# Optimization experiments

Measured on AMD Instinct MI355X. Metric: run time of the kernel, lower is better.

The kernel has to match this reference:

```python
import jax, jax.numpy as jnp
import numpy as np

G, N, F, H, L, B = 8, 1024, 128, 256, 4, 64


def setup_inputs() -> dict:
    key = jax.random.key(0)
    ks = jax.random.split(key, 8)
    graph = jax.random.randint(ks[0], (B,), 0, G)
    # boolean coverpoint mask; force column 0 True so no row is empty
    mask = jax.random.uniform(ks[1], (B, N)) < 0.2
    mask = mask.at[:, 0].set(True)
    cdfg_xs = jax.random.normal(ks[2], (G, N, F), dtype=jnp.float32)
    cdfg_as = (jax.random.uniform(ks[3], (G, N, N)) < 0.02).astype(jnp.float32) / 20.0
    W_in = jax.random.normal(ks[4], (F, H), dtype=jnp.float32) * (1.0 / np.sqrt(F))
    b_in = jnp.zeros((H,), dtype=jnp.float32)
    Ws = jax.random.normal(ks[5], (L, H, H), dtype=jnp.float32) * (1.0 / np.sqrt(H))
    bs = jnp.zeros((L, H), dtype=jnp.float32)
    return {"graph": graph, "coverpoint_mask": mask, "cdfg_xs": cdfg_xs,
            "cdfg_as": cdfg_as, "W_in": W_in, "b_in": b_in, "Ws": Ws, "bs": bs}


def reference(graph, coverpoint_mask, cdfg_xs, cdfg_as, W_in, b_in, Ws, bs):
    # gather per-sample graphs (tf.gather_nd equivalent)
    xs = cdfg_xs[graph]          # [B, N, F]
    As = cdfg_as[graph]          # [B, N, N]
    # input Dense with relu
    x = jax.nn.relu(jnp.einsum('bnf,fh->bnh', xs, W_in) + b_in)  # [B, N, H]
    to_add = x
    n_layers = Ws.shape[0]
    for i in range(n_layers):
        h = jnp.einsum('bnm,bmh->bnh', As, jnp.einsum('bnh,hk->bnk', x, Ws[i])) + bs[i]
        if i == n_layers - 1:
            x = jax.nn.softmax(h, axis=-1)   # final_activation='softmax'
        else:
            x = jax.nn.relu(h)
    x = x + to_add
    # ragged boolean_mask + reduce_mean over nodes == masked mean
    m = coverpoint_mask[..., None].astype(x.dtype)   # [B, N, 1]
    s = jnp.sum(x * m, axis=1)                       # [B, H]
    cnt = jnp.maximum(jnp.sum(m, axis=1), 1.0)
    return s / cnt
```

## Files before the change

### kernel.cpp

```cpp
#include <hip/hip_runtime.h>
#include <hip/hip_bf16.h>

#define GG 8
#define NN 1024
#define FF 128
#define HH 256
#define LL 4
#define BB 64
#define MM (GG * NN)
#define ELLCAP 96

typedef __attribute__((ext_vector_type(8))) short bf16x8_t;
typedef __attribute__((ext_vector_type(4))) float f32x4_t;

__device__ inline unsigned short f2bf(float f) {
  union { float f; unsigned u; } c;
  c.f = f;
  unsigned r = (c.u + 0x7fffu + ((c.u >> 16) & 1u)) >> 16;
  return (unsigned short)r;
}
__device__ inline float bf2f(unsigned short u) {
  union { unsigned u; float f; } c;
  c.u = (unsigned)u << 16;
  return c.f;
}

#define PB_DET 16
#define PB_XS (PB_DET + 1024)
#define PB_W (PB_XS + 1152)
#define PB_ELL (PB_W + 2048)
__global__ __launch_bounds__(256) void prep_kernel(
    const uint4* __restrict__ mask4, int* __restrict__ flags,
    const float4* __restrict__ xs4, ushort4* __restrict__ xsb4,
    const float* __restrict__ W_in, const float* __restrict__ Ws,
    unsigned short* __restrict__ WinT, unsigned short* __restrict__ WsT,
    const float* __restrict__ Adj, uint2* __restrict__ ell,
    int* __restrict__ cntArr) {
  const int bx = blockIdx.x;
  if (bx < PB_DET) {
    const int i = bx * 256 + threadIdx.x;
    const uint4 v = mask4[i];
    const unsigned all = v.x | v.y | v.z | v.w;
    const int nonz = (all & 0xFFFFFF00u) != 0;
    const int isf32 = ((v.x >> 24) == 0x3fu) || ((v.y >> 24) == 0x3fu) ||
                      ((v.z >> 24) == 0x3fu) || ((v.w >> 24) == 0x3fu);
    const unsigned long long bn = __ballot(nonz);
    const unsigned long long bf = __ballot(isf32);
    if ((threadIdx.x & 63) == 0) {
      if (bn) atomicOr(&flags[0], 1);
      if (bf) atomicOr(&flags[1], 1);
    }
  } else if (bx < PB_XS) {
    const int i = (bx - PB_DET) * 256 + threadIdx.x;
    const float4 v = xs4[i];
    ushort4 o;
    o.x = f2bf(v.x); o.y = f2bf(v.y); o.z = f2bf(v.z); o.w = f2bf(v.w);
    xsb4[i] = o;
  } else if (bx < PB_W) {
    const int idx = (bx - PB_XS) * 256 + threadIdx.x;
    if (idx < FF * HH) {
      const int n = idx >> 7, k = idx & (FF - 1);
      WinT[idx] = f2bf(W_in[k * HH + n]);
    } else {
      const int j = idx - FF * HH;
      const int l = j >> 16, n = (j >> 8) & 255, k = j & 255;
      WsT[j] = f2bf(Ws[((size_t)l * HH + k) * HH + n]);
    }
  } else {
    const int lane = threadIdx.x & 63;
    const int wid = threadIdx.x >> 6;
    const int r = (bx - PB_W) * 4 + wid;
    const float* __restrict__ Arow = Adj + (size_t)r * NN;
    int cnt = 0;
    for (int mc = 0; mc < NN; mc += 64) {
      const float a = Arow[mc + lane];
      const unsigned long long bal = __ballot(a != 0.0f);
      if (a != 0.0f) {
        const int pos = cnt + __popcll(bal & ((1ULL << lane) - 1ULL));
        if (pos < ELLCAP) {
          uint2 e;
          e.x = __float_as_uint(a);
          e.y = (unsigned)(mc + lane);
          ell[(size_t)r * ELLCAP + pos] = e;
        }
      }
      cnt += __popcll(bal);
    }
    if (lane == 0) cntArr[r] = min(cnt, ELLCAP);
  }
}

template <int K, bool FUSED>
__global__ __launch_bounds__(256) void mfma_gemm_kernel(
    const unsigned short* __restrict__ A, const unsigned short* __restrict__ BT,
    const float* __restrict__ bias, unsigned short* __restrict__ Cb,
    float* __restrict__ Cf) {
  constexpr int KS = K / 8;
  __shared__ uint4 As4[64 * KS];
  __shared__ uint4 Bs4[64 * KS];
  const int t = threadIdx.x;
  const int lane = t & 63;
  const int w = t >> 6;
  const int wm = (w >> 1) * 32;
  const int wn = (w & 1) * 32;
  const int m0 = blockIdx.x * 64;
  const int n0 = blockIdx.y * 64;
  const int lk = lane >> 4;
  const int lr = lane & 15;
  const uint4* __restrict__ Ag = (const uint4*)(A + (size_t)m0 * K);
  const uint4* __restrict__ Bg = (const uint4*)(BT + (size_t)n0 * K);
#pragma unroll
  for (int it = 0; it < K / 32; ++it) {
    const int c = it * 256 + t;
    const int row = c / KS;
    const int k = c % KS;
    const int slot = row * KS + (k ^ (row & 7));
    As4[slot] = Ag[c];
    Bs4[slot] = Bg[c];
  }
  __syncthreads();
  f32x4_t acc[2][2] = {};
#pragma unroll
  for (int ks = 0; ks < K / 32; ++ks) {
    const int q = ks * 4 + lk;
    const int ra0 = wm + lr, ra1 = wm + 16 + lr;
    const int rb0 = wn + lr, rb1 = wn + 16 + lr;
    const bf16x8_t a0 = *(const bf16x8_t*)(&As4[ra0 * KS + (q ^ (ra0 & 7))]);
    const bf16x8_t a1 = *(const bf16x8_t*)(&As4[ra1 * KS + (q ^ (ra1 & 7))]);
    const bf16x8_t b0 = *(const bf16x8_t*)(&Bs4[rb0 * KS + (q ^ (rb0 & 7))]);
    const bf16x8_t b1 = *(const bf16x8_t*)(&Bs4[rb1 * KS + (q ^ (rb1 & 7))]);
    acc[0][0] = __builtin_amdgcn_mfma_f32_16x16x32_bf16(a0, b0, acc[0][0], 0, 0, 0);
    acc[0][1] = __builtin_amdgcn_mfma_f32_16x16x32_bf16(a0, b1, acc[0][1], 0, 0, 0);
    acc[1][0] = __builtin_amdgcn_mfma_f32_16x16x32_bf16(a1, b0, acc[1][0], 0, 0, 0);
    acc[1][1] = __builtin_amdgcn_mfma_f32_16x16x32_bf16(a1, b1, acc[1][1], 0, 0, 0);
  }
#pragma unroll
  for (int rg = 0; rg < 2; ++rg)
#pragma unroll
    for (int cg = 0; cg < 2; ++cg)
#pragma unroll
      for (int j = 0; j < 4; ++j) {
        const int row = m0 + wm + rg * 16 + (lane >> 4) * 4 + j;
        const int col = n0 + wn + cg * 16 + lr;
        float v = acc[rg][cg][j];
        if (FUSED) {
          v += bias[col];
          v = fmaxf(v, 0.0f);
          Cb[(size_t)row * HH + col] = f2bf(v);
          Cf[(size_t)row * HH + col] = v;
        } else {
          Cb[(size_t)row * HH + col] = f2bf(v);
        }
      }
}

__global__ __launch_bounds__(256) void spmm_ell_kernel(
    const uint2* __restrict__ ell, const int* __restrict__ cntArr,
    const unsigned short* __restrict__ Yb, const float* __restrict__ bias,
    const float* __restrict__ X0, unsigned short* __restrict__ Xb,
    float* __restrict__ Xf, int final_layer) {
  const int lane = threadIdx.x & 63;
  const int wid = threadIdx.x >> 6;
  const int r = blockIdx.x * 4 + wid;
  const int g = r >> 10;
  const unsigned short* __restrict__ Yg = Yb + (size_t)g * NN * HH;
  const int cnt = cntArr[r];
  const uint2* __restrict__ erow = ell + (size_t)r * ELLCAP;
  float p0 = 0.f, p1 = 0.f, p2 = 0.f, p3 = 0.f;
  float q0 = 0.f, q1 = 0.f, q2 = 0.f, q3 = 0.f;
  for (int base = 0; base < cnt; base += 64) {
    const int m = min(64, cnt - base);
    const uint2 e = erow[base + ((lane < m) ? lane : 0)];
    int j = 0;
    for (; j + 2 <= m; j += 2) {
      const float v0 = __uint_as_float(__shfl(e.x, j));
      const int i0 = (int)__shfl(e.y, j);
      const float v1 = __uint_as_float(__shfl(e.x, j + 1));
      const int i1 = (int)__shfl(e.y, j + 1);
      const ushort4 y0 = *(const ushort4*)(Yg + (size_t)i0 * HH + lane * 4);
      const ushort4 y1 = *(const ushort4*)(Yg + (size_t)i1 * HH + lane * 4);
      p0 += v0 * bf2f(y0.x); p1 += v0 * bf2f(y0.y);
      p2 += v0 * bf2f(y0.z); p3 += v0 * bf2f(y0.w);
      q0 += v1 * bf2f(y1.x); q1 += v1 * bf2f(y1.y);
      q2 += v1 * bf2f(y1.z); q3 += v1 * bf2f(y1.w);
    }
    if (j < m) {
      const float v0 = __uint_as_float(__shfl(e.x, j));
      const int i0 = (int)__shfl(e.y, j);
      const ushort4 y0 = *(const ushort4*)(Yg + (size_t)i0 * HH + lane * 4);
      p0 += v0 * bf2f(y0.x); p1 += v0 * bf2f(y0.y);
      p2 += v0 * bf2f(y0.z); p3 += v0 * bf2f(y0.w);
    }
  }
  const float4 b4 = *(const float4*)(bias + lane * 4);
  const float h0 = p0 + q0 + b4.x, h1 = p1 + q1 + b4.y;
  const float h2 = p2 + q2 + b4.z, h3 = p3 + q3 + b4.w;
  const size_t rowoff = (size_t)r * HH;
  if (!final_layer) {
    ushort4 o;
    o.x = f2bf(fmaxf(h0, 0.f));
    o.y = f2bf(fmaxf(h1, 0.f));
    o.z = f2bf(fmaxf(h2, 0.f));
    o.w = f2bf(fmaxf(h3, 0.f));
    *(ushort4*)(Xb + rowoff + lane * 4) = o;
  } else {
    float mx = fmaxf(fmaxf(h0, h1), fmaxf(h2, h3));
#pragma unroll
    for (int off = 32; off >= 1; off >>= 1) mx = fmaxf(mx, __shfl_xor(mx, off));
    const float e0 = __expf(h0 - mx), e1 = __expf(h1 - mx);
    const float e2 = __expf(h2 - mx), e3 = __expf(h3 - mx);
    float s = e0 + e1 + e2 + e3;
#pragma unroll
    for (int off = 32; off >= 1; off >>= 1) s += __shfl_xor(s, off);
    const float inv = 1.0f / s;
    const float4 x0 = *(const float4*)(X0 + rowoff + lane * 4);
    float4 o;
    o.x = e0 * inv + x0.x;
    o.y = e1 * inv + x0.y;
    o.z = e2 * inv + x0.z;
    o.w = e3 * inv + x0.w;
    *(float4*)(Xf + rowoff + lane * 4) = o;
  }
}

__global__ __launch_bounds__(256) void mm_partial_kernel(
    const float* __restrict__ X, const int* __restrict__ graph,
    const void* __restrict__ mask, const int* __restrict__ flags,
    float* __restrict__ partial, float* __restrict__ cntbuf) {
  __shared__ unsigned char m[64];
  const int c = blockIdx.x;
  const int b = blockIdx.y;
  const int h = threadIdx.x;
  const int n0 = c * 64;
  const int mode = flags[1] ? 2 : (flags[0] ? 0 : 1);
  if (h < 64) {
    const int n = n0 + h;
    bool on;
    if (mode == 1) on = ((const int*)mask)[(size_t)b * NN + n] != 0;
    else if (mode == 2) on = ((const float*)mask)[(size_t)b * NN + n] != 0.0f;
    else on = ((const unsigned char*)mask)[(size_t)b * NN + n] != 0;
    m[h] = on ? 1 : 0;
  }
  __syncthreads();
  const int g = graph[b];
  const float* __restrict__ Xg = X + ((size_t)g * NN + n0) * HH;
  float a0 = 0.f, a1 = 0.f, a2 = 0.f, a3 = 0.f;
  int c0 = 0, c1 = 0, c2 = 0, c3 = 0;
#pragma unroll 4
  for (int n = 0; n < 16; ++n) {
    if (m[n])      { a0 += Xg[(size_t)n * HH + h]; c0++; }
    if (m[n + 16]) { a1 += Xg[(size_t)(n + 16) * HH + h]; c1++; }
    if (m[n + 32]) { a2 += Xg[(size_t)(n + 32) * HH + h]; c2++; }
    if (m[n + 48]) { a3 += Xg[(size_t)(n + 48) * HH + h]; c3++; }
  }
  partial[((size_t)b * 16 + c) * HH + h] = (a0 + a1) + (a2 + a3);
  if (h == 0) cntbuf[b * 16 + c] = (float)((c0 + c1) + (c2 + c3));
}

__global__ __launch_bounds__(256) void mm_reduce_kernel(
    const float* __restrict__ partial, const float* __restrict__ cntbuf,
    float* __restrict__ out) {
  const int b = blockIdx.x, h = threadIdx.x;
  float s = 0.f;
#pragma unroll
  for (int c = 0; c < 16; ++c) s += partial[((size_t)b * 16 + c) * HH + h];
  float cnt = 0.f;
#pragma unroll
  for (int c = 0; c < 16; ++c) cnt += cntbuf[b * 16 + c];
  out[(size_t)b * HH + h] = s / fmaxf(cnt, 1.0f);
}

extern "C" void kernel_launch(void* const* d_in, const int* in_sizes, int n_in,
                              void* d_out, int out_size, void* d_ws,
                              size_t ws_size, hipStream_t stream) {
  const int* graph = (const int*)d_in[0];
  const void* mask = d_in[1];
  const float* xs = (const float*)d_in[2];
  const float* As = (const float*)d_in[3];
  const float* W_in = (const float*)d_in[4];
  const float* b_in = (const float*)d_in[5];
  const float* Ws = (const float*)d_in[6];
  const float* bs = (const float*)d_in[7];
  float* out = (float*)d_out;

  float* X = (float*)d_ws;
  float* X0 = X + (size_t)MM * HH;
  unsigned short* Yb = (unsigned short*)(X0 + (size_t)MM * HH);
  unsigned short* Xb = Yb + (size_t)MM * HH;
  unsigned short* xsb = Xb + (size_t)MM * HH;
  unsigned short* WinT = xsb + (size_t)MM * FF;
  unsigned short* WsT = WinT + (size_t)HH * FF;
  uint2* ell = (uint2*)(WsT + (size_t)LL * HH * HH);
  int* cntArr = (int*)(ell + (size_t)MM * ELLCAP);
  int* flags = cntArr + MM;
  float* partial = (float*)(flags + 2);
  float* cntbuf = partial + (size_t)BB * 16 * HH;

  hipMemsetAsync(flags, 0, 2 * sizeof(int), stream);
  prep_kernel<<<PB_ELL, 256, 0, stream>>>(
      (const uint4*)mask, flags, (const float4*)xs, (ushort4*)xsb, W_in, Ws,
      WinT, WsT, As, ell, cntArr);

  const dim3 grd(MM / 64, HH / 64);
  mfma_gemm_kernel<FF, true><<<grd, 256, 0, stream>>>(xsb, WinT, b_in, Xb, X0);
  for (int i = 0; i < LL; ++i) {
    mfma_gemm_kernel<HH, false><<<grd, 256, 0, stream>>>(
        Xb, WsT + (size_t)i * HH * HH, nullptr, Yb, nullptr);
    spmm_ell_kernel<<<MM / 4, 256, 0, stream>>>(
        ell, cntArr, Yb, bs + (size_t)i * HH, X0, Xb, X, (i == LL - 1) ? 1 : 0);
  }
  mm_partial_kernel<<<dim3(16, BB), 256, 0, stream>>>(X, graph, mask, flags,
                                                      partial, cntbuf);
  mm_reduce_kernel<<<BB, 256, 0, stream>>>(partial, cntbuf, out);
}
```

Baseline: 185.5 us.

## Fuse all stages into one cooperative persistent kernel with grid syncs

Replaces the sequence of separate launches (prep, input GEMM, per-layer GEMM and SpMM, masked-mean partial and reduce, plus a memset) with a single cooperative kernel of 256 persistent blocks. The blocks loop over virtual tiles and use grid-wide syncs between stages. Mask-type detection now runs in one block with shared-memory flags instead of global atomics across 16 blocks. This removes launch gaps and the memset, but with only 256 blocks the GEMM and SpMM stages get less parallelism and occupancy, since 64KB of shared memory per block limits residency. It also adds the cost of the grid barriers.

```diff
diff --git a/kernel.cpp b/kernel.cpp
--- a/kernel.cpp
+++ b/kernel.cpp
@@ -1,5 +1,7 @@
 #include <hip/hip_runtime.h>
-#include <hip/hip_bf16.h>
+#include <hip/hip_cooperative_groups.h>
+
+namespace cg = cooperative_groups;
 
 #define GG 8
 #define NN 1024
@@ -9,6 +11,12 @@
 #define BB 64
 #define MM (GG * NN)
 #define ELLCAP 96
+#define NBLK 256
+
+#define PB_DET 1
+#define PB_XS (PB_DET + 1024)
+#define PB_W (PB_XS + 1152)
+#define PB_TOT (PB_W + 2048)
 
 typedef __attribute__((ext_vector_type(8))) short bf16x8_t;
 typedef __attribute__((ext_vector_type(4))) float f32x4_t;
@@ -25,90 +33,51 @@
   return c.f;
 }
 
-#define PB_DET 16
-#define PB_XS (PB_DET + 1024)
-#define PB_W (PB_XS + 1152)
-#define PB_ELL (PB_W + 2048)
-__global__ __launch_bounds__(256) void prep_kernel(
-    const uint4* __restrict__ mask4, int* __restrict__ flags,
-    const float4* __restrict__ xs4, ushort4* __restrict__ xsb4,
-    const float* __restrict__ W_in, const float* __restrict__ Ws,
-    unsigned short* __restrict__ WinT, unsigned short* __restrict__ WsT,
-    const float* __restrict__ Adj, uint2* __restrict__ ell,
-    int* __restrict__ cntArr) {
-  const int bx = blockIdx.x;
-  if (bx < PB_DET) {
-    const int i = bx * 256 + threadIdx.x;
-    const uint4 v = mask4[i];
-    const unsigned all = v.x | v.y | v.z | v.w;
-    const int nonz = (all & 0xFFFFFF00u) != 0;
-    const int isf32 = ((v.x >> 24) == 0x3fu) || ((v.y >> 24) == 0x3fu) ||
-                      ((v.z >> 24) == 0x3fu) || ((v.w >> 24) == 0x3fu);
-    const unsigned long long bn = __ballot(nonz);
-    const unsigned long long bf = __ballot(isf32);
-    if ((threadIdx.x & 63) == 0) {
-      if (bn) atomicOr(&flags[0], 1);
-      if (bf) atomicOr(&flags[1], 1);
-    }
-  } else if (bx < PB_XS) {
-    const int i = (bx - PB_DET) * 256 + threadIdx.x;
-    const float4 v = xs4[i];
-    ushort4 o;
-    o.x = f2bf(v.x); o.y = f2bf(v.y); o.z = f2bf(v.z); o.w = f2bf(v.w);
-    xsb4[i] = o;
-  } else if (bx < PB_W) {
-    const int idx = (bx - PB_XS) * 256 + threadIdx.x;
-    if (idx < FF * HH) {
-      const int n = idx >> 7, k = idx & (FF - 1);
-      WinT[idx] = f2bf(W_in[k * HH + n]);
-    } else {
-      const int j = idx - FF * HH;
-      const int l = j >> 16, n = (j >> 8) & 255, k = j & 255;
-      WsT[j] = f2bf(Ws[((size_t)l * HH + k) * HH + n]);
-    }
-  } else {
-    const int lane = threadIdx.x & 63;
-    const int wid = threadIdx.x >> 6;
-    const int r = (bx - PB_W) * 4 + wid;
-    const float* __restrict__ Arow = Adj + (size_t)r * NN;
-    int cnt = 0;
-    for (int mc = 0; mc < NN; mc += 64) {
-      const float a = Arow[mc + lane];
-      const unsigned long long bal = __ballot(a != 0.0f);
-      if (a != 0.0f) {
-        const int pos = cnt + __popcll(bal & ((1ULL << lane) - 1ULL));
-        if (pos < ELLCAP) {
-          uint2 e;
-          e.x = __float_as_uint(a);
-          e.y = (unsigned)(mc + lane);
-          ell[(size_t)r * ELLCAP + pos] = e;
-        }
-      }
-      cnt += __popcll(bal);
-    }
-    if (lane == 0) cntArr[r] = min(cnt, ELLCAP);
-  }
-}
+struct KParams {
+  const int* graph;
+  const void* mask;
+  const float* xs;
+  const float* Adj;
+  const float* W_in;
+  const float* b_in;
+  const float* Ws;
+  const float* bs;
+  float* out;
+  float* X;
+  float* X0;
+  unsigned short* Yb;
+  unsigned short* Xb;
+  unsigned short* xsb;
+  unsigned short* WinT;
+  unsigned short* WsT;
+  uint2* ell;
+  int* cntArr;
+  int* flags;
+  float* partial;
+  float* cntbuf;
+};
 
 template <int K, bool FUSED>
-__global__ __launch_bounds__(256) void mfma_gemm_kernel(
-    const unsigned short* __restrict__ A, const unsigned short* __restrict__ BT,
-    const float* __restrict__ bias, unsigned short* __restrict__ Cb,
-    float* __restrict__ Cf) {
+__device__ inline void gemm_tile(const unsigned short* __restrict__ A,
+                                 const unsigned short* __restrict__ BT,
+                                 const float* __restrict__ bias,
+                                 unsigned short* __restrict__ Cb,
+                                 float* __restrict__ Cf, uint4* smem, int vt,
+                                 int t) {
   constexpr int KS = K / 8;
-  __shared__ uint4 As4[64 * KS];
-  __shared__ uint4 Bs4[64 * KS];
-  const int t = threadIdx.x;
+  uint4* As4 = smem;
+  uint4* Bs4 = smem + 64 * KS;
   const int lane = t & 63;
   const int w = t >> 6;
   const int wm = (w >> 1) * 32;
   const int wn = (w & 1) * 32;
-  const int m0 = blockIdx.x * 64;
-  const int n0 = blockIdx.y * 64;
+  const int m0 = (vt >> 2) * 64;
+  const int n0 = (vt & 3) * 64;
   const int lk = lane >> 4;
   const int lr = lane & 15;
   const uint4* __restrict__ Ag = (const uint4*)(A + (size_t)m0 * K);
   const uint4* __restrict__ Bg = (const uint4*)(BT + (size_t)n0 * K);
+  __syncthreads();
 #pragma unroll
   for (int it = 0; it < K / 32; ++it) {
     const int c = it * 256 + t;
@@ -154,162 +123,228 @@
       }
 }
 
-__global__ __launch_bounds__(256) void spmm_ell_kernel(
-    const uint2* __restrict__ ell, const int* __restrict__ cntArr,
-    const unsigned short* __restrict__ Yb, const float* __restrict__ bias,
-    const float* __restrict__ X0, unsigned short* __restrict__ Xb,
-    float* __restrict__ Xf, int final_layer) {
-  const int lane = threadIdx.x & 63;
-  const int wid = threadIdx.x >> 6;
-  const int r = blockIdx.x * 4 + wid;
-  const int g = r >> 10;
-  const unsigned short* __restrict__ Yg = Yb + (size_t)g * NN * HH;
-  const int cnt = cntArr[r];
-  const uint2* __restrict__ erow = ell + (size_t)r * ELLCAP;
-  float p0 = 0.f, p1 = 0.f, p2 = 0.f, p3 = 0.f;
-  float q0 = 0.f, q1 = 0.f, q2 = 0.f, q3 = 0.f;
-  for (int base = 0; base < cnt; base += 64) {
-    const int m = min(64, cnt - base);
-    const uint2 e = erow[base + ((lane < m) ? lane : 0)];
-    int j = 0;
-    for (; j + 2 <= m; j += 2) {
-      const float v0 = __uint_as_float(__shfl(e.x, j));
-      const int i0 = (int)__shfl(e.y, j);
-      const float v1 = __uint_as_float(__shfl(e.x, j + 1));
-      const int i1 = (int)__shfl(e.y, j + 1);
-      const ushort4 y0 = *(const ushort4*)(Yg + (size_t)i0 * HH + lane * 4);
-      const ushort4 y1 = *(const ushort4*)(Yg + (size_t)i1 * HH + lane * 4);
-      p0 += v0 * bf2f(y0.x); p1 += v0 * bf2f(y0.y);
-      p2 += v0 * bf2f(y0.z); p3 += v0 * bf2f(y0.w);
-      q0 += v1 * bf2f(y1.x); q1 += v1 * bf2f(y1.y);
-      q2 += v1 * bf2f(y1.z); q3 += v1 * bf2f(y1.w);
+__global__ __launch_bounds__(256) void fused_kernel(KParams p) {
+  cg::grid_group grid = cg::this_grid();
+  __shared__ uint4 smem[4096];
+  const int bid = blockIdx.x;
+  const int t = threadIdx.x;
+  const int lane = t & 63;
+  const int wid = t >> 6;
+
+  for (int vb = bid; vb < PB_TOT; vb += NBLK) {
+    if (vb == 0) {
+      int* df = (int*)smem;
+      if (t < 2) df[t] = 0;
+      __syncthreads();
+      int nonz = 0, isf = 0;
+      const uint4* mask4 = (const uint4*)p.mask;
+      for (int i = t; i < 4096; i += 256) {
+        const uint4 v = mask4[i];
+        const unsigned all = v.x | v.y | v.z | v.w;
+        if (all & 0xFFFFFF00u) nonz = 1;
+        if (((v.x >> 24) == 0x3fu) || ((v.y >> 24) == 0x3fu) ||
+            ((v.z >> 24) == 0x3fu) || ((v.w >> 24) == 0x3fu))
+          isf = 1;
+      }
+      if (nonz) atomicOr(&df[0], 1);
+      if (isf) atomicOr(&df[1], 1);
+      __syncthreads();
+      if (t == 0) p.flags[0] = df[1] ? 2 : (df[0] ? 0 : 1);
+      __syncthreads();
+    } else if (vb < PB_XS) {
+      const int i = (vb - PB_DET) * 256 + t;
+      const float4 v = ((const float4*)p.xs)[i];
+      ushort4 o;
+      o.x = f2bf(v.x); o.y = f2bf(v.y); o.z = f2bf(v.z); o.w = f2bf(v.w);
+      ((ushort4*)p.xsb)[i] = o;
+    } else if (vb < PB_W) {
+      const int idx = (vb - PB_XS) * 256 + t;
+      if (idx < FF * HH) {
+        const int n = idx >> 7, k = idx & (FF - 1);
+        p.WinT[idx] = f2bf(p.W_in[k * HH + n]);
+      } else {
+        const int j = idx - FF * HH;
+        const int l = j >> 16, n = (j >> 8) & 255, k = j & 255;
+        p.WsT[j] = f2bf(p.Ws[((size_t)l * HH + k) * HH + n]);
+      }
+    } else {
+      const int r = (vb - PB_W) * 4 + wid;
+      const float* __restrict__ Arow = p.Adj + (size_t)r * NN;
+      int cnt = 0;
+      for (int mc = 0; mc < NN; mc += 64) {
+        const float a = Arow[mc + lane];
+        const unsigned long long bal = __ballot(a != 0.0f);
+        if (a != 0.0f) {
+          const int pos = cnt + __popcll(bal & ((1ULL << lane) - 1ULL));
+          if (pos < ELLCAP) {
+            uint2 e;
+            e.x = __float_as_uint(a);
+            e.y = (unsigned)(mc + lane);
+            p.ell[(size_t)r * ELLCAP + pos] = e;
+          }
+        }
+        cnt += __popcll(bal);
+      }
+      if (lane == 0) p.cntArr[r] = min(cnt, ELLCAP);
     }
-    if (j < m) {
-      const float v0 = __uint_as_float(__shfl(e.x, j));
-      const int i0 = (int)__shfl(e.y, j);
-      const ushort4 y0 = *(const ushort4*)(Yg + (size_t)i0 * HH + lane * 4);
-      p0 += v0 * bf2f(y0.x); p1 += v0 * bf2f(y0.y);
-      p2 += v0 * bf2f(y0.z); p3 += v0 * bf2f(y0.w);
+  }
+  grid.sync();
+
+  for (int vt = bid; vt < 512; vt += NBLK)
+    gemm_tile<FF, true>(p.xsb, p.WinT, p.b_in, p.Xb, p.X0, smem, vt, t);
+  grid.sync();
+
+  for (int i = 0; i < LL; ++i) {
+    for (int vt = bid; vt < 512; vt += NBLK)
+      gemm_tile<HH, false>(p.Xb, p.WsT + (size_t)i * HH * HH, nullptr, p.Yb,
+                           nullptr, smem, vt, t);
+    grid.sync();
+    {
+      const int fin = (i == LL - 1);
+      const float* __restrict__ bias = p.bs + (size_t)i * HH;
+      for (int vt = bid; vt < 2048; vt += NBLK) {
+        const int r = vt * 4 + wid;
+        const int g = r >> 10;
+        const unsigned short* __restrict__ Yg = p.Yb + (size_t)g * NN * HH;
+        const int cnt = p.cntArr[r];
+        const uint2* __restrict__ erow = p.ell + (size_t)r * ELLCAP;
+        float p0 = 0.f, p1 = 0.f, p2 = 0.f, p3 = 0.f;
+        float q0 = 0.f, q1 = 0.f, q2 = 0.f, q3 = 0.f;
+        for (int base = 0; base < cnt; base += 64) {
+          const int m = min(64, cnt - base);
+          const uint2 e = erow[base + ((lane < m) ? lane : 0)];
+          int j = 0;
+          for (; j + 2 <= m; j += 2) {
+            const float v0 = __uint_as_float(__shfl(e.x, j));
+            const int i0 = (int)__shfl(e.y, j);
+            const float v1 = __uint_as_float(__shfl(e.x, j + 1));
+            const int i1 = (int)__shfl(e.y, j + 1);
+            const ushort4 y0 =
+                *(const ushort4*)(Yg + (size_t)i0 * HH + (lane << 2));
+            const ushort4 y1 =
+                *(const ushort4*)(Yg + (size_t)i1 * HH + (lane << 2));
+            p0 += v0 * bf2f(y0.x); p1 += v0 * bf2f(y0.y);
+            p2 += v0 * bf2f(y0.z); p3 += v0 * bf2f(y0.w);
+            q0 += v1 * bf2f(y1.x); q1 += v1 * bf2f(y1.y);
+            q2 += v1 * bf2f(y1.z); q3 += v1 * bf2f(y1.w);
+          }
+          if (j < m) {
+            const float v0 = __uint_as_float(__shfl(e.x, j));
+            const int i0 = (int)__shfl(e.y, j);
+            const ushort4 y0 =
+                *(const ushort4*)(Yg + (size_t)i0 * HH + (lane << 2));
+            p0 += v0 * bf2f(y0.x); p1 += v0 * bf2f(y0.y);
+            p2 += v0 * bf2f(y0.z); p3 += v0 * bf2f(y0.w);
+          }
+        }
+        const float4 b4 = *(const float4*)(bias + (lane << 2));
+        const float h0 = p0 + q0 + b4.x, h1 = p1 + q1 + b4.y;
+        const float h2 = p2 + q2 + b4.z, h3 = p3 + q3 + b4.w;
+        const size_t rowoff = (size_t)r * HH;
+        if (!fin) {
+          ushort4 o;
+          o.x = f2bf(fmaxf(h0, 0.f));
+          o.y = f2bf(fmaxf(h1, 0.f));
+          o.z = f2bf(fmaxf(h2, 0.f));
+          o.w = f2bf(fmaxf(h3, 0.f));
+          *(ushort4*)(p.Xb + rowoff + (lane << 2)) = o;
+        } else {
+          float mx = fmaxf(fmaxf(h0, h1), fmaxf(h2, h3));
+#pragma unroll
+          for (int off = 32; off >= 1; off >>= 1)
+            mx = fmaxf(mx, __shfl_xor(mx, off));
+          const float e0 = __expf(h0 - mx), e1 = __expf(h1 - mx);
+          const float e2 = __expf(h2 - mx), e3 = __expf(h3 - mx);
+          float s = e0 + e1 + e2 + e3;
+#pragma unroll
+          for (int off = 32; off >= 1; off >>= 1) s += __shfl_xor(s, off);
+          const float inv = 1.0f / s;
+          const float4 x0 = *(const float4*)(p.X0 + rowoff + (lane << 2));
+          float4 o;
+          o.x = e0 * inv + x0.x;
+          o.y = e1 * inv + x0.y;
+          o.z = e2 * inv + x0.z;
+          o.w = e3 * inv + x0.w;
+          *(float4*)(p.X + rowoff + (lane << 2)) = o;
+        }
+      }
     }
-  }
-  const float4 b4 = *(const float4*)(bias + lane * 4);
-  const float h0 = p0 + q0 + b4.x, h1 = p1 + q1 + b4.y;
-  const float h2 = p2 + q2 + b4.z, h3 = p3 + q3 + b4.w;
-  const size_t rowoff = (size_t)r * HH;
-  if (!final_layer) {
-    ushort4 o;
-    o.x = f2bf(fmaxf(h0, 0.f));
-    o.y = f2bf(fmaxf(h1, 0.f));
-    o.z = f2bf(fmaxf(h2, 0.f));
-    o.w = f2bf(fmaxf(h3, 0.f));
-    *(ushort4*)(Xb + rowoff + lane * 4) = o;
-  } else {
-    float mx = fmaxf(fmaxf(h0, h1), fmaxf(h2, h3));
-#pragma unroll
-    for (int off = 32; off >= 1; off >>= 1) mx = fmaxf(mx, __shfl_xor(mx, off));
-    const float e0 = __expf(h0 - mx), e1 = __expf(h1 - mx);
-    const float e2 = __expf(h2 - mx), e3 = __expf(h3 - mx);
-    float s = e0 + e1 + e2 + e3;
-#pragma unroll
-    for (int off = 32; off >= 1; off >>= 1) s += __shfl_xor(s, off);
-    const float inv = 1.0f / s;
-    const float4 x0 = *(const float4*)(X0 + rowoff + lane * 4);
-    float4 o;
-    o.x = e0 * inv + x0.x;
-    o.y = e1 * inv + x0.y;
-    o.z = e2 * inv + x0.z;
-    o.w = e3 * inv + x0.w;
-    *(float4*)(Xf + rowoff + lane * 4) = o;
-  }
-}
-
-__global__ __launch_bounds__(256) void mm_partial_kernel(
-    const float* __restrict__ X, const int* __restrict__ graph,
-    const void* __restrict__ mask, const int* __restrict__ flags,
-    float* __restrict__ partial, float* __restrict__ cntbuf) {
-  __shared__ unsigned char m[64];
-  const int c = blockIdx.x;
-  const int b = blockIdx.y;
-  const int h = threadIdx.x;
-  const int n0 = c * 64;
-  const int mode = flags[1] ? 2 : (flags[0] ? 0 : 1);
-  if (h < 64) {
-    const int n = n0 + h;
-    bool on;
-    if (mode == 1) on = ((const int*)mask)[(size_t)b * NN + n] != 0;
-    else if (mode == 2) on = ((const float*)mask)[(size_t)b * NN + n] != 0.0f;
-    else on = ((const unsigned char*)mask)[(size_t)b * NN + n] != 0;
-    m[h] = on ? 1 : 0;
-  }
-  __syncthreads();
-  const int g = graph[b];
-  const float* __restrict__ Xg = X + ((size_t)g * NN + n0) * HH;
-  float a0 = 0.f, a1 = 0.f, a2 = 0.f, a3 = 0.f;
-  int c0 = 0, c1 = 0, c2 = 0, c3 = 0;
+    grid.sync();
+  }
+
+  {
+    unsigned char* m = (unsigned char*)smem;
+    const int mode = p.flags[0];
+    for (int vb = bid; vb < 16 * BB; vb += NBLK) {
+      const int c = vb & 15, b = vb >> 4;
+      const int n0 = c * 64;
+      __syncthreads();
+      if (t < 64) {
+        const int n = n0 + t;
+        bool on;
+        if (mode == 1) on = ((const int*)p.mask)[(size_t)b * NN + n] != 0;
+        else if (mode == 2) on = ((const float*)p.mask)[(size_t)b * NN + n] != 0.0f;
+        else on = ((const unsigned char*)p.mask)[(size_t)b * NN + n] != 0;
+        m[t] = on ? 1 : 0;
+      }
+      __syncthreads();
+      const int g = p.graph[b];
+      const float* __restrict__ Xg = p.X + ((size_t)g * NN + n0) * HH;
+      float a0 = 0.f, a1 = 0.f, a2 = 0.f, a3 = 0.f;
+      int c0 = 0, c1 = 0, c2 = 0, c3 = 0;
 #pragma unroll 4
-  for (int n = 0; n < 16; ++n) {
-    if (m[n])      { a0 += Xg[(size_t)n * HH + h]; c0++; }
-    if (m[n + 16]) { a1 += Xg[(size_t)(n + 16) * HH + h]; c1++; }
-    if (m[n + 32]) { a2 += Xg[(size_t)(n + 32) * HH + h]; c2++; }
-    if (m[n + 48]) { a3 += Xg[(size_t)(n + 48) * HH + h]; c3++; }
-  }
-  partial[((size_t)b * 16 + c) * HH + h] = (a0 + a1) + (a2 + a3);
-  if (h == 0) cntbuf[b * 16 + c] = (float)((c0 + c1) + (c2 + c3));
-}
-
-__global__ __launch_bounds__(256) void mm_reduce_kernel(
-    const float* __restrict__ partial, const float* __restrict__ cntbuf,
-    float* __restrict__ out) {
-  const int b = blockIdx.x, h = threadIdx.x;
-  float s = 0.f;
-#pragma unroll
-  for (int c = 0; c < 16; ++c) s += partial[((size_t)b * 16 + c) * HH + h];
-  float cnt = 0.f;
-#pragma unroll
-  for (int c = 0; c < 16; ++c) cnt += cntbuf[b * 16 + c];
-  out[(size_t)b * HH + h] = s / fmaxf(cnt, 1.0f);
+      for (int n = 0; n < 16; ++n) {
+        if (m[n])      { a0 += Xg[(size_t)n * HH + t]; c0++; }
+        if (m[n + 16]) { a1 += Xg[(size_t)(n + 16) * HH + t]; c1++; }
+        if (m[n + 32]) { a2 += Xg[(size_t)(n + 32) * HH + t]; c2++; }
+        if (m[n + 48]) { a3 += Xg[(size_t)(n + 48) * HH + t]; c3++; }
+      }
+      p.partial[((size_t)b * 16 + c) * HH + t] = (a0 + a1) + (a2 + a3);
+      if (t == 0) p.cntbuf[b * 16 + c] = (float)((c0 + c1) + (c2 + c3));
+    }
+  }
+  grid.sync();
+
+  if (bid < BB) {
+    const int b = bid;
+    float s = 0.f;
+#pragma unroll
+    for (int c = 0; c < 16; ++c) s += p.partial[((size_t)b * 16 + c) * HH + t];
+    float cnt = 0.f;
+#pragma unroll
+    for (int c = 0; c < 16; ++c) cnt += p.cntbuf[b * 16 + c];
+    p.out[(size_t)b * HH + t] = s / fmaxf(cnt, 1.0f);
+  }
 }
 
 extern "C" void kernel_launch(void* const* d_in, const int* in_sizes, int n_in,
                               void* d_out, int out_size, void* d_ws,
                               size_t ws_size, hipStream_t stream) {
-  const int* graph = (const int*)d_in[0];
-  const void* mask = d_in[1];
-  const float* xs = (const float*)d_in[2];
-  const float* As = (const float*)d_in[3];
-  const float* W_in = (const float*)d_in[4];
-  const float* b_in = (const float*)d_in[5];
-  const float* Ws = (const float*)d_in[6];
-  const float* bs = (const float*)d_in[7];
-  float* out = (float*)d_out;
-
-  float* X = (float*)d_ws;
-  float* X0 = X + (size_t)MM * HH;
-  unsigned short* Yb = (unsigned short*)(X0 + (size_t)MM * HH);
-  unsigned short* Xb = Yb + (size_t)MM * HH;
-  unsigned short* xsb = Xb + (size_t)MM * HH;
-  unsigned short* WinT = xsb + (size_t)MM * FF;
-  unsigned short* WsT = WinT + (size_t)HH * FF;
-  uint2* ell = (uint2*)(WsT + (size_t)LL * HH * HH);
-  int* cntArr = (int*)(ell + (size_t)MM * ELLCAP);
-  int* flags = cntArr + MM;
-  float* partial = (float*)(flags + 2);
-  float* cntbuf = partial + (size_t)BB * 16 * HH;
-
-  hipMemsetAsync(flags, 0, 2 * sizeof(int), stream);
-  prep_kernel<<<PB_ELL, 256, 0, stream>>>(
-      (const uint4*)mask, flags, (const float4*)xs, (ushort4*)xsb, W_in, Ws,
-      WinT, WsT, As, ell, cntArr);
-
-  const dim3 grd(MM / 64, HH / 64);
-  mfma_gemm_kernel<FF, true><<<grd, 256, 0, stream>>>(xsb, WinT, b_in, Xb, X0);
-  for (int i = 0; i < LL; ++i) {
-    mfma_gemm_kernel<HH, false><<<grd, 256, 0, stream>>>(
-        Xb, WsT + (size_t)i * HH * HH, nullptr, Yb, nullptr);
-    spmm_ell_kernel<<<MM / 4, 256, 0, stream>>>(
-        ell, cntArr, Yb, bs + (size_t)i * HH, X0, Xb, X, (i == LL - 1) ? 1 : 0);
-  }
-  mm_partial_kernel<<<dim3(16, BB), 256, 0, stream>>>(X, graph, mask, flags,
-                                                      partial, cntbuf);
-  mm_reduce_kernel<<<BB, 256, 0, stream>>>(partial, cntbuf, out);
-}
+  KParams p;
+  p.graph = (const int*)d_in[0];
+  p.mask = d_in[1];
+  p.xs = (const float*)d_in[2];
+  p.Adj = (const float*)d_in[3];
+  p.W_in = (const float*)d_in[4];
+  p.b_in = (const float*)d_in[5];
+  p.Ws = (const float*)d_in[6];
+  p.bs = (const float*)d_in[7];
+  p.out = (float*)d_out;
+
+  p.X = (float*)d_ws;
+  p.X0 = p.X + (size_t)MM * HH;
+  p.Yb = (unsigned short*)(p.X0 + (size_t)MM * HH);
+  p.Xb = p.Yb + (size_t)MM * HH;
+  p.xsb = p.Xb + (size_t)MM * HH;
+  p.WinT = p.xsb + (size_t)MM * FF;
+  p.WsT = p.WinT + (size_t)HH * FF;
+  p.ell = (uint2*)(p.WsT + (size_t)LL * HH * HH);
+  p.cntArr = (int*)(p.ell + (size_t)MM * ELLCAP);
+  p.flags = p.cntArr + MM;
+  p.partial = (float*)(p.flags + 2);
+  p.cntbuf = p.partial + (size_t)BB * 16 * HH;
+
+  void* args[] = {&p};
+  hipLaunchCooperativeKernel((void*)fused_kernel, dim3(NBLK), dim3(256), args,
+                             0, stream);
+}
```

After: 691.6 us. 3.73x slower.

## Fuse sparse aggregation and dense GEMM per layer using reassociated A(XW)

Applied to the files above, without the earlier changes.

Each GCN layer now computes (A·X)·W instead of A·(X·W). It does this in a single kernel: it gathers ELL neighbours into a 16-row bf16 tile in LDS, then multiplies by the streamed W with MFMA. Bias and ReLU are applied in the epilogue. This removes the separate GEMM launch and the Yb round trip per layer. In exchange, every 16-row block reloads the full 256x256 weight matrix, and the final softmax plus residual moves to a separate kernel that reads an fp32 H buffer. Mask-type detection also moves into one block that writes a mode flag, dropping the memset and the atomics.

```diff
diff --git a/kernel.cpp b/kernel.cpp
--- a/kernel.cpp
+++ b/kernel.cpp
@@ -25,10 +25,6 @@
   return c.f;
 }
 
-#define PB_DET 16
-#define PB_XS (PB_DET + 1024)
-#define PB_W (PB_XS + 1152)
-#define PB_ELL (PB_W + 2048)
 __global__ __launch_bounds__(256) void prep_kernel(
     const uint4* __restrict__ mask4, int* __restrict__ flags,
     const float4* __restrict__ xs4, ushort4* __restrict__ xsb4,
@@ -37,27 +33,32 @@
     const float* __restrict__ Adj, uint2* __restrict__ ell,
     int* __restrict__ cntArr) {
   const int bx = blockIdx.x;
-  if (bx < PB_DET) {
-    const int i = bx * 256 + threadIdx.x;
-    const uint4 v = mask4[i];
-    const unsigned all = v.x | v.y | v.z | v.w;
-    const int nonz = (all & 0xFFFFFF00u) != 0;
-    const int isf32 = ((v.x >> 24) == 0x3fu) || ((v.y >> 24) == 0x3fu) ||
-                      ((v.z >> 24) == 0x3fu) || ((v.w >> 24) == 0x3fu);
-    const unsigned long long bn = __ballot(nonz);
-    const unsigned long long bf = __ballot(isf32);
-    if ((threadIdx.x & 63) == 0) {
-      if (bn) atomicOr(&flags[0], 1);
-      if (bf) atomicOr(&flags[1], 1);
-    }
-  } else if (bx < PB_XS) {
-    const int i = (bx - PB_DET) * 256 + threadIdx.x;
+  const int t = threadIdx.x;
+  if (bx == 0) {
+    __shared__ int df[2];
+    if (t < 2) df[t] = 0;
+    __syncthreads();
+    int nonz = 0, isf = 0;
+    for (int i = t; i < 4096; i += 256) {
+      const uint4 v = mask4[i];
+      const unsigned all = v.x | v.y | v.z | v.w;
+      if (all & 0xFFFFFF00u) nonz = 1;
+      if (((v.x >> 24) == 0x3fu) || ((v.y >> 24) == 0x3fu) ||
+          ((v.z >> 24) == 0x3fu) || ((v.w >> 24) == 0x3fu))
+        isf = 1;
+    }
+    if (nonz) atomicOr(&df[0], 1);
+    if (isf) atomicOr(&df[1], 1);
+    __syncthreads();
+    if (t == 0) flags[0] = df[1] ? 2 : (df[0] ? 0 : 1);
+  } else if (bx < 1025) {
+    const int i = (bx - 1) * 256 + t;
     const float4 v = xs4[i];
     ushort4 o;
     o.x = f2bf(v.x); o.y = f2bf(v.y); o.z = f2bf(v.z); o.w = f2bf(v.w);
     xsb4[i] = o;
-  } else if (bx < PB_W) {
-    const int idx = (bx - PB_XS) * 256 + threadIdx.x;
+  } else if (bx < 2177) {
+    const int idx = (bx - 1025) * 256 + t;
     if (idx < FF * HH) {
       const int n = idx >> 7, k = idx & (FF - 1);
       WinT[idx] = f2bf(W_in[k * HH + n]);
@@ -67,9 +68,9 @@
       WsT[j] = f2bf(Ws[((size_t)l * HH + k) * HH + n]);
     }
   } else {
-    const int lane = threadIdx.x & 63;
-    const int wid = threadIdx.x >> 6;
-    const int r = (bx - PB_W) * 4 + wid;
+    const int lane = t & 63;
+    const int wid = t >> 6;
+    const int r = (bx - 2177) * 4 + wid;
     const float* __restrict__ Arow = Adj + (size_t)r * NN;
     int cnt = 0;
     for (int mc = 0; mc < NN; mc += 64) {
@@ -90,12 +91,11 @@
   }
 }
 
-template <int K, bool FUSED>
-__global__ __launch_bounds__(256) void mfma_gemm_kernel(
+__global__ __launch_bounds__(256) void input_gemm_kernel(
     const unsigned short* __restrict__ A, const unsigned short* __restrict__ BT,
     const float* __restrict__ bias, unsigned short* __restrict__ Cb,
     float* __restrict__ Cf) {
-  constexpr int KS = K / 8;
+  constexpr int K = FF, KS = K / 8;
   __shared__ uint4 As4[64 * KS];
   __shared__ uint4 Bs4[64 * KS];
   const int t = threadIdx.x;
@@ -142,85 +142,128 @@
       for (int j = 0; j < 4; ++j) {
         const int row = m0 + wm + rg * 16 + (lane >> 4) * 4 + j;
         const int col = n0 + wn + cg * 16 + lr;
-        float v = acc[rg][cg][j];
-        if (FUSED) {
-          v += bias[col];
-          v = fmaxf(v, 0.0f);
-          Cb[(size_t)row * HH + col] = f2bf(v);
-          Cf[(size_t)row * HH + col] = v;
-        } else {
-          Cb[(size_t)row * HH + col] = f2bf(v);
-        }
-      }
-}
-
-__global__ __launch_bounds__(256) void spmm_ell_kernel(
+        float v = acc[rg][cg][j] + bias[col];
+        v = fmaxf(v, 0.0f);
+        Cb[(size_t)row * HH + col] = f2bf(v);
+        Cf[(size_t)row * HH + col] = v;
+      }
+}
+
+template <bool FINAL>
+__global__ __launch_bounds__(256) void layer_kernel(
     const uint2* __restrict__ ell, const int* __restrict__ cntArr,
-    const unsigned short* __restrict__ Yb, const float* __restrict__ bias,
-    const float* __restrict__ X0, unsigned short* __restrict__ Xb,
-    float* __restrict__ Xf, int final_layer) {
+    const unsigned short* __restrict__ Xin, const unsigned short* __restrict__ WT,
+    const float* __restrict__ bias, unsigned short* __restrict__ Xout,
+    float* __restrict__ Hout) {
+  __shared__ __align__(16) unsigned short Z[16][264];
+  __shared__ uint4 Wl[256 * 8];
+  const int t = threadIdx.x;
+  const int lane = t & 63;
+  const int w = t >> 6;
+  const int r0 = blockIdx.x * 16;
+  const int g = r0 >> 10;
+  const unsigned short* __restrict__ Xg = Xin + (size_t)g * NN * HH;
+
+  for (int rr = w * 4; rr < w * 4 + 4; ++rr) {
+    const int r = r0 + rr;
+    const int cnt = cntArr[r];
+    const uint2* __restrict__ erow = ell + (size_t)r * ELLCAP;
+    float p0 = 0.f, p1 = 0.f, p2 = 0.f, p3 = 0.f;
+    float q0 = 0.f, q1 = 0.f, q2 = 0.f, q3 = 0.f;
+    for (int base = 0; base < cnt; base += 64) {
+      const int m = min(64, cnt - base);
+      const uint2 e = erow[base + ((lane < m) ? lane : 0)];
+      int j = 0;
+      for (; j + 2 <= m; j += 2) {
+        const float v0 = __uint_as_float(__shfl(e.x, j));
+        const int i0 = (int)__shfl(e.y, j);
+        const float v1 = __uint_as_float(__shfl(e.x, j + 1));
+        const int i1 = (int)__shfl(e.y, j + 1);
+        const ushort4 y0 = *(const ushort4*)(Xg + (size_t)i0 * HH + (lane << 2));
+        const ushort4 y1 = *(const ushort4*)(Xg + (size_t)i1 * HH + (lane << 2));
+        p0 += v0 * bf2f(y0.x); p1 += v0 * bf2f(y0.y);
+        p2 += v0 * bf2f(y0.z); p3 += v0 * bf2f(y0.w);
+        q0 += v1 * bf2f(y1.x); q1 += v1 * bf2f(y1.y);
+        q2 += v1 * bf2f(y1.z); q3 += v1 * bf2f(y1.w);
+      }
+      if (j < m) {
+        const float v0 = __uint_as_float(__shfl(e.x, j));
+        const int i0 = (int)__shfl(e.y, j);
+        const ushort4 y0 = *(const ushort4*)(Xg + (size_t)i0 * HH + (lane << 2));
+        p0 += v0 * bf2f(y0.x); p1 += v0 * bf2f(y0.y);
+        p2 += v0 * bf2f(y0.z); p3 += v0 * bf2f(y0.w);
+      }
+    }
+    ushort4 z;
+    z.x = f2bf(p0 + q0); z.y = f2bf(p1 + q1);
+    z.z = f2bf(p2 + q2); z.w = f2bf(p3 + q3);
+    *(ushort4*)&Z[rr][lane << 2] = z;
+  }
+  __syncthreads();
+
+  const int lr = lane & 15;
+  const int lk = lane >> 4;
+  f32x4_t acc[4] = {};
+  for (int kc = 0; kc < 4; ++kc) {
+    if (kc) __syncthreads();
+#pragma unroll
+    for (int it = 0; it < 8; ++it) {
+      const int c = it * 256 + t;
+      const int n = c >> 3, k8 = c & 7;
+      Wl[n * 8 + (k8 ^ (n & 7))] = ((const uint4*)WT)[n * 32 + kc * 8 + k8];
+    }
+    __syncthreads();
+#pragma unroll
+    for (int ks = 0; ks < 2; ++ks) {
+      const bf16x8_t a = *(const bf16x8_t*)&Z[lr][kc * 64 + ks * 32 + lk * 8];
+      const int k8 = ks * 4 + lk;
+#pragma unroll
+      for (int nt = 0; nt < 4; ++nt) {
+        const int n = w * 64 + nt * 16 + lr;
+        const bf16x8_t b = *(const bf16x8_t*)&Wl[n * 8 + (k8 ^ (n & 7))];
+        acc[nt] = __builtin_amdgcn_mfma_f32_16x16x32_bf16(a, b, acc[nt], 0, 0, 0);
+      }
+    }
+  }
+#pragma unroll
+  for (int nt = 0; nt < 4; ++nt)
+#pragma unroll
+    for (int j = 0; j < 4; ++j) {
+      const int row = r0 + lk * 4 + j;
+      const int col = w * 64 + nt * 16 + lr;
+      const float v = acc[nt][j] + bias[col];
+      if (FINAL)
+        Hout[(size_t)row * HH + col] = v;
+      else
+        Xout[(size_t)row * HH + col] = f2bf(fmaxf(v, 0.0f));
+    }
+}
+
+__global__ __launch_bounds__(256) void softmax_res_kernel(
+    const float* __restrict__ H, const float* __restrict__ X0,
+    float* __restrict__ X) {
   const int lane = threadIdx.x & 63;
   const int wid = threadIdx.x >> 6;
   const int r = blockIdx.x * 4 + wid;
-  const int g = r >> 10;
-  const unsigned short* __restrict__ Yg = Yb + (size_t)g * NN * HH;
-  const int cnt = cntArr[r];
-  const uint2* __restrict__ erow = ell + (size_t)r * ELLCAP;
-  float p0 = 0.f, p1 = 0.f, p2 = 0.f, p3 = 0.f;
-  float q0 = 0.f, q1 = 0.f, q2 = 0.f, q3 = 0.f;
-  for (int base = 0; base < cnt; base += 64) {
-    const int m = min(64, cnt - base);
-    const uint2 e = erow[base + ((lane < m) ? lane : 0)];
-    int j = 0;
-    for (; j + 2 <= m; j += 2) {
-      const float v0 = __uint_as_float(__shfl(e.x, j));
-      const int i0 = (int)__shfl(e.y, j);
-      const float v1 = __uint_as_float(__shfl(e.x, j + 1));
-      const int i1 = (int)__shfl(e.y, j + 1);
-      const ushort4 y0 = *(const ushort4*)(Yg + (size_t)i0 * HH + lane * 4);
-      const ushort4 y1 = *(const ushort4*)(Yg + (size_t)i1 * HH + lane * 4);
-      p0 += v0 * bf2f(y0.x); p1 += v0 * bf2f(y0.y);
-      p2 += v0 * bf2f(y0.z); p3 += v0 * bf2f(y0.w);
-      q0 += v1 * bf2f(y1.x); q1 += v1 * bf2f(y1.y);
-      q2 += v1 * bf2f(y1.z); q3 += v1 * bf2f(y1.w);
-    }
-    if (j < m) {
-      const float v0 = __uint_as_float(__shfl(e.x, j));
-      const int i0 = (int)__shfl(e.y, j);
-      const ushort4 y0 = *(const ushort4*)(Yg + (size_t)i0 * HH + lane * 4);
-      p0 += v0 * bf2f(y0.x); p1 += v0 * bf2f(y0.y);
-      p2 += v0 * bf2f(y0.z); p3 += v0 * bf2f(y0.w);
-    }
-  }
-  const float4 b4 = *(const float4*)(bias + lane * 4);
-  const float h0 = p0 + q0 + b4.x, h1 = p1 + q1 + b4.y;
-  const float h2 = p2 + q2 + b4.z, h3 = p3 + q3 + b4.w;
   const size_t rowoff = (size_t)r * HH;
-  if (!final_layer) {
-    ushort4 o;
-    o.x = f2bf(fmaxf(h0, 0.f));
-    o.y = f2bf(fmaxf(h1, 0.f));
-    o.z = f2bf(fmaxf(h2, 0.f));
-    o.w = f2bf(fmaxf(h3, 0.f));
-    *(ushort4*)(Xb + rowoff + lane * 4) = o;
-  } else {
-    float mx = fmaxf(fmaxf(h0, h1), fmaxf(h2, h3));
-#pragma unroll
-    for (int off = 32; off >= 1; off >>= 1) mx = fmaxf(mx, __shfl_xor(mx, off));
-    const float e0 = __expf(h0 - mx), e1 = __expf(h1 - mx);
-    const float e2 = __expf(h2 - mx), e3 = __expf(h3 - mx);
-    float s = e0 + e1 + e2 + e3;
-#pragma unroll
-    for (int off = 32; off >= 1; off >>= 1) s += __shfl_xor(s, off);
-    const float inv = 1.0f / s;
-    const float4 x0 = *(const float4*)(X0 + rowoff + lane * 4);
-    float4 o;
-    o.x = e0 * inv + x0.x;
-    o.y = e1 * inv + x0.y;
-    o.z = e2 * inv + x0.z;
-    o.w = e3 * inv + x0.w;
-    *(float4*)(Xf + rowoff + lane * 4) = o;
-  }
+  const float4 h4 = *(const float4*)(H + rowoff + (lane << 2));
+  const float h0 = h4.x, h1 = h4.y, h2 = h4.z, h3 = h4.w;
+  float mx = fmaxf(fmaxf(h0, h1), fmaxf(h2, h3));
+#pragma unroll
+  for (int off = 32; off >= 1; off >>= 1) mx = fmaxf(mx, __shfl_xor(mx, off));
+  const float e0 = __expf(h0 - mx), e1 = __expf(h1 - mx);
+  const float e2 = __expf(h2 - mx), e3 = __expf(h3 - mx);
+  float s = e0 + e1 + e2 + e3;
+#pragma unroll
+  for (int off = 32; off >= 1; off >>= 1) s += __shfl_xor(s, off);
+  const float inv = 1.0f / s;
+  const float4 x0 = *(const float4*)(X0 + rowoff + (lane << 2));
+  float4 o;
+  o.x = e0 * inv + x0.x;
+  o.y = e1 * inv + x0.y;
+  o.z = e2 * inv + x0.z;
+  o.w = e3 * inv + x0.w;
+  *(float4*)(X + rowoff + (lane << 2)) = o;
 }
 
 __global__ __launch_bounds__(256) void mm_partial_kernel(
@@ -232,7 +275,7 @@
   const int b = blockIdx.y;
   const int h = threadIdx.x;
   const int n0 = c * 64;
-  const int mode = flags[1] ? 2 : (flags[0] ? 0 : 1);
+  const int mode = flags[0];
   if (h < 64) {
     const int n = n0 + h;
     bool on;
@@ -296,19 +339,20 @@
   float* partial = (float*)(flags + 2);
   float* cntbuf = partial + (size_t)BB * 16 * HH;
 
-  hipMemsetAsync(flags, 0, 2 * sizeof(int), stream);
-  prep_kernel<<<PB_ELL, 256, 0, stream>>>(
-      (const uint4*)mask, flags, (const float4*)xs, (ushort4*)xsb, W_in, Ws,
-      WinT, WsT, As, ell, cntArr);
-
-  const dim3 grd(MM / 64, HH / 64);
-  mfma_gemm_kernel<FF, true><<<grd, 256, 0, stream>>>(xsb, WinT, b_in, Xb, X0);
-  for (int i = 0; i < LL; ++i) {
-    mfma_gemm_kernel<HH, false><<<grd, 256, 0, stream>>>(
-        Xb, WsT + (size_t)i * HH * HH, nullptr, Yb, nullptr);
-    spmm_ell_kernel<<<MM / 4, 256, 0, stream>>>(
-        ell, cntArr, Yb, bs + (size_t)i * HH, X0, Xb, X, (i == LL - 1) ? 1 : 0);
-  }
+  prep_kernel<<<4225, 256, 0, stream>>>((const uint4*)mask, flags,
+                                        (const float4*)xs, (ushort4*)xsb, W_in,
+                                        Ws, WinT, WsT, As, ell, cntArr);
+  input_gemm_kernel<<<dim3(MM / 64, HH / 64), 256, 0, stream>>>(xsb, WinT, b_in,
+                                                                Xb, X0);
+  layer_kernel<false><<<MM / 16, 256, 0, stream>>>(ell, cntArr, Xb, WsT, bs, Yb,
+                                                   nullptr);
+  layer_kernel<false><<<MM / 16, 256, 0, stream>>>(
+      ell, cntArr, Yb, WsT + (size_t)HH * HH, bs + HH, Xb, nullptr);
+  layer_kernel<false><<<MM / 16, 256, 0, stream>>>(
+      ell, cntArr, Xb, WsT + (size_t)2 * HH * HH, bs + 2 * HH, Yb, nullptr);
+  layer_kernel<true><<<MM / 16, 256, 0, stream>>>(
+      ell, cntArr, Yb, WsT + (size_t)3 * HH * HH, bs + 3 * HH, nullptr, X);
+  softmax_res_kernel<<<MM / 4, 256, 0, stream>>>(X, X0, X);
   mm_partial_kernel<<<dim3(16, BB), 256, 0, stream>>>(X, graph, mask, flags,
                                                       partial, cntbuf);
   mm_reduce_kernel<<<BB, 256, 0, stream>>>(partial, cntbuf, out);
```

New measurement: 222.6 us. 1.2x slower.
